# Performance work log

Measured on AMD Instinct MI355X. Metric: run time of the kernel, lower is better.

Reference implementation:

```python
import jax, jax.numpy as jnp
import numpy as np

B, N, E = 32, 2000, 32000      # graphs, nodes/graph, edges/graph
V, D, R, K = 100000, 128, 39, 8  # vocab, emb_dim, n_relation, n_bases
EPS = 1e-5


def setup_inputs() -> dict:
    key = jax.random.key(0)
    ks = jax.random.split(key, 8)
    node_ids = jax.random.randint(ks[0], (B, N), 0, V)
    edge_index = jax.random.randint(ks[1], (B, 2, E), 0, N)
    edge_type = jax.random.randint(ks[2], (B, E), 0, R)
    embedding = jax.random.normal(ks[3], (V, D), jnp.float32) * D ** -0.5
    bases = jax.random.normal(ks[4], (K, D, D), jnp.float32) * D ** -0.5
    comp = jax.random.normal(ks[5], (R, K), jnp.float32) * K ** -0.5
    root = jax.random.normal(ks[6], (D, D), jnp.float32) * D ** -0.5
    bias = jnp.zeros((D,), jnp.float32)
    return dict(node_ids=node_ids, edge_index=edge_index, edge_type=edge_type,
                embedding=embedding, bases=bases, comp=comp, root=root, bias=bias)


def _graph_fwd(node_ids, edge_index, edge_type, embedding, bases, comp, root, bias):
    # RGCNConv with basis decomposition and per-relation MEAN aggregation (PyG default).
    x = embedding[node_ids]                       # [N, D] per-graph node features
    src, dst = edge_index[0], edge_index[1]       # j -> i, aggregate at dst
    x_src = x[src]                                # [E, D]
    # mean normalizer per (dst, relation) bucket
    comb = dst * R + edge_type                    # [E]
    cnt = jax.ops.segment_sum(jnp.ones((E,), jnp.float32), comb, num_segments=N * R)
    inv = jnp.where(cnt > 0, 1.0 / cnt, 0.0)[comb]  # [E]
    # W_r = sum_k comp[r,k] * bases[k]; fold comp coefficients + mean norm into edge weights
    w = comp[edge_type] * inv[:, None]            # [E, K]
    out = x @ root + bias                         # root/self connection
    for k in range(K):                            # small fixed loop over bases
        zk = jax.ops.segment_sum(w[:, k:k + 1] * x_src, dst, num_segments=N)  # [N, D]
        out = out + zk @ bases[k]
    g = out.sum(axis=0)                           # sum pool over nodes
    # torch.nn.functional.normalize(p=2, eps=1e-5)
    return g / jnp.maximum(jnp.linalg.norm(g), EPS)


def reference(node_ids, edge_index, edge_type, embedding, bases, comp, root, bias):
    f = jax.vmap(_graph_fwd, in_axes=(0, 0, 0, None, None, None, None, None))
    return f(node_ids, edge_index, edge_type, embedding, bases, comp, root, bias)  # [B, D]
```

## Files before the change

### kernel.cpp

```cpp
#include <hip/hip_runtime.h>
#include <math.h>

#define Bn 32
#define Nn 2000
#define En 32000
#define Vn 100000
#define Dn 128
#define Rn 39
#define Kn 8

#define SUBS 8
#define NPS (Nn / SUBS)
#define WPG 64
#define NPAIR (Nn / 2)
#define EQ (En / 4)
#define NR (NPS * Rn)


__global__ __launch_bounds__(1024) void cntinv_kernel(const int* __restrict__ edge_index,
                                                      const int* __restrict__ edge_type,
                                                      float* __restrict__ inv) {
    int b = blockIdx.x, sub = blockIdx.y;
    int base = sub * NR;
    __shared__ int loc[NR];
    for (int i = threadIdx.x; i < NR; i += 1024) loc[i] = 0;
    __syncthreads();
    const int4* dst4 = (const int4*)(edge_index + (b * 2 + 1) * En);
    const int4* et4  = (const int4*)(edge_type + b * En);
    for (int q = threadIdx.x; q < EQ; q += 1024) {
        int4 d = dst4[q]; int4 t = et4[q]; int y;
        y = d.x * Rn + t.x - base; if ((unsigned)y < NR) atomicAdd(&loc[y], 1);
        y = d.y * Rn + t.y - base; if ((unsigned)y < NR) atomicAdd(&loc[y], 1);
        y = d.z * Rn + t.z - base; if ((unsigned)y < NR) atomicAdd(&loc[y], 1);
        y = d.w * Rn + t.w - base; if ((unsigned)y < NR) atomicAdd(&loc[y], 1);
    }
    __syncthreads();
    float* ivb = inv + (size_t)b * En;
    for (int q = threadIdx.x; q < EQ; q += 1024) {
        int4 d = dst4[q]; int4 t = et4[q];
        int e = 4 * q, y;
        y = d.x * Rn + t.x - base; if ((unsigned)y < NR) ivb[e]     = 1.0f / (float)loc[y];
        y = d.y * Rn + t.y - base; if ((unsigned)y < NR) ivb[e + 1] = 1.0f / (float)loc[y];
        y = d.z * Rn + t.z - base; if ((unsigned)y < NR) ivb[e + 2] = 1.0f / (float)loc[y];
        y = d.w * Rn + t.w - base; if ((unsigned)y < NR) ivb[e + 3] = 1.0f / (float)loc[y];
    }
}

__global__ __launch_bounds__(1024) void a_kernel(const int* __restrict__ edge_index,
                                                 const int* __restrict__ edge_type,
                                                 const float* __restrict__ inv,
                                                 const float* __restrict__ comp,
                                                 float* __restrict__ a) {
    int b = blockIdx.x, sub = blockIdx.y;
    int base = sub * NR;
    __shared__ float s[NR];
    __shared__ float comp_l[Rn * Kn];
    for (int i = threadIdx.x; i < NR; i += 1024) s[i] = 0.0f;
    if (threadIdx.x < Rn * Kn) comp_l[threadIdx.x] = comp[threadIdx.x];
    __syncthreads();
    const int4*   src4 = (const int4*)(edge_index + (b * 2 + 0) * En);
    const int4*   et4  = (const int4*)(edge_type + b * En);
    const float4* iv4  = (const float4*)(inv + (size_t)b * En);
    for (int q = threadIdx.x; q < EQ; q += 1024) {
        int4 sv = src4[q]; int4 tv = et4[q]; float4 iv = iv4[q]; int y;
        y = sv.x * Rn + tv.x - base; if ((unsigned)y < NR) atomicAdd(&s[y], iv.x);
        y = sv.y * Rn + tv.y - base; if ((unsigned)y < NR) atomicAdd(&s[y], iv.y);
        y = sv.z * Rn + tv.z - base; if ((unsigned)y < NR) atomicAdd(&s[y], iv.z);
        y = sv.w * Rn + tv.w - base; if ((unsigned)y < NR) atomicAdd(&s[y], iv.w);
    }
    __syncthreads();
    float* g = a + ((size_t)b * Nn + sub * NPS) * Kn;
    for (int i = threadIdx.x; i < NPS * Kn; i += 1024) {
        int n = i >> 3, k = i & 7;
        float acc = 0.0f;
        const float* srow = &s[n * Rn];
        for (int t = 0; t < Rn; t++) acc += srow[t] * comp_l[t * Kn + k];
        g[i] = acc;
    }
}

__global__ __launch_bounds__(256) void gather_kernel(const int* __restrict__ node_ids,
                                                     const float* __restrict__ emb,
                                                     const float* __restrict__ a,
                                                     float* __restrict__ partial) {
    int b = blockIdx.x;
    int lane = threadIdx.x & 63, wv = threadIdx.x >> 6;
    int W = blockIdx.y * 4 + wv;
    int half = lane >> 5;
    int dl = lane & 31;
    float4 acc[9];
#pragma unroll
    for (int k = 0; k < 9; k++) acc[k] = make_float4(0.f, 0.f, 0.f, 0.f);
    const int*   nb = node_ids + b * Nn;
    const float* ab = a + (size_t)b * Nn * Kn;
    for (int p0 = W; p0 < NPAIR; p0 += 8 * WPG) {
        bool   has[8];
        int    node[8];
        float4 v[8];
        float4 a0[8], a1[8];
#pragma unroll
        for (int i = 0; i < 8; i++) {
            int p = p0 + i * WPG;
            has[i] = p < NPAIR;
            node[i] = (has[i] ? 2 * p : 0) + half;
        }
#pragma unroll
        for (int i = 0; i < 8; i++) {
            int nid = nb[node[i]];
            v[i] = has[i] ? ((const float4*)(emb + (size_t)nid * Dn))[dl]
                          : make_float4(0.f, 0.f, 0.f, 0.f);
            const float4* ar = (const float4*)(ab + (size_t)node[i] * Kn);
            a0[i] = ar[0]; a1[i] = ar[1];
        }
#pragma unroll
        for (int i = 0; i < 8; i++) {
            float w[9] = {a0[i].x, a0[i].y, a0[i].z, a0[i].w,
                          a1[i].x, a1[i].y, a1[i].z, a1[i].w, 1.0f};
#pragma unroll
            for (int k = 0; k < 9; k++) {
                acc[k].x += w[k] * v[i].x;
                acc[k].y += w[k] * v[i].y;
                acc[k].z += w[k] * v[i].z;
                acc[k].w += w[k] * v[i].w;
            }
        }
    }
#pragma unroll
    for (int k = 0; k < 9; k++) {
        acc[k].x += __shfl_down(acc[k].x, 32, 64);
        acc[k].y += __shfl_down(acc[k].y, 32, 64);
        acc[k].z += __shfl_down(acc[k].z, 32, 64);
        acc[k].w += __shfl_down(acc[k].w, 32, 64);
    }
    if (half == 0) {
#pragma unroll
        for (int k = 0; k < 9; k++) {
            float4* gp = (float4*)(partial + (((size_t)b * 9 + k) * WPG + W) * Dn);
            gp[dl] = acc[k];
        }
    }
}

__global__ __launch_bounds__(256) void matvec_kernel(const float* __restrict__ partial,
                                                     const float* __restrict__ root,
                                                     const float* __restrict__ bases,
                                                     float* __restrict__ gmat) {
    int b = blockIdx.x, m = blockIdx.y;
    int tid = threadIdx.x;
    __shared__ float4 ts4[Dn / 4];
    __shared__ float tsh[8][Dn];
    int dg = tid & 31, part = tid >> 5;
    const float4* p4 = (const float4*)(partial + ((size_t)b * 9 + m) * WPG * Dn);
    float4 sum = make_float4(0.f, 0.f, 0.f, 0.f);
    for (int c = part; c < WPG; c += 8) {
        float4 v = p4[c * 32 + dg];
        sum.x += v.x; sum.y += v.y; sum.z += v.z; sum.w += v.w;
    }
    ((float4*)tsh[part])[dg] = sum;
    __syncthreads();
    if (part == 0) {
        float4 t = make_float4(0.f, 0.f, 0.f, 0.f);
#pragma unroll
        for (int r = 0; r < 8; r++) {
            float4 v = ((float4*)tsh[r])[dg];
            t.x += v.x; t.y += v.y; t.z += v.z; t.w += v.w;
        }
        ts4[dg] = t;
    }
    __syncthreads();
    const float* ts = (const float*)ts4;
    const float* M  = (m == 8) ? root : bases + (size_t)m * Dn * Dn;
    int d = tid & (Dn - 1), h = tid >> 7;
    float g = 0.0f;
    for (int j = h * 64; j < h * 64 + 64; j++) g += ts[j] * M[j * Dn + d];
    __syncthreads();
    tsh[h][d] = g;
    __syncthreads();
    if (h == 0) gmat[((size_t)b * 9 + m) * Dn + d] = tsh[0][d] + tsh[1][d];
}

__global__ __launch_bounds__(128) void norm_kernel(const float* __restrict__ gmat,
                                                   const float* __restrict__ bias,
                                                   float* __restrict__ out) {
    int b = blockIdx.x, d = threadIdx.x;
    float g = (float)Nn * bias[d];
    const float* gb = gmat + (size_t)b * 9 * Dn + d;
#pragma unroll
    for (int m = 0; m < 9; m++) g += gb[m * Dn];
    float ss = g * g;
#pragma unroll
    for (int off = 32; off > 0; off >>= 1) ss += __shfl_down(ss, off, 64);
    __shared__ float s2[2];
    if ((threadIdx.x & 63) == 0) s2[threadIdx.x >> 6] = ss;
    __syncthreads();
    float nrm = sqrtf(s2[0] + s2[1]);
    out[b * Dn + d] = g / fmaxf(nrm, 1e-5f);
}

extern "C" void kernel_launch(void* const* d_in, const int* in_sizes, int n_in,
                              void* d_out, int out_size, void* d_ws, size_t ws_size,
                              hipStream_t stream) {
    const int*   node_ids   = (const int*)d_in[0];
    const int*   edge_index = (const int*)d_in[1];
    const int*   edge_type  = (const int*)d_in[2];
    const float* embedding  = (const float*)d_in[3];
    const float* bases      = (const float*)d_in[4];
    const float* comp       = (const float*)d_in[5];
    const float* root       = (const float*)d_in[6];
    const float* bias       = (const float*)d_in[7];
    float*       out        = (float*)d_out;

    char* w = (char*)d_ws;
    float* inv     = (float*)(w + 0);
    float* a       = (float*)(w + 4096000);
    float* partial = (float*)(w + 6144000);
    float* gmat    = (float*)(w + 15581184);

    cntinv_kernel<<<dim3(Bn, SUBS),    1024, 0, stream>>>(edge_index, edge_type, inv);
    a_kernel     <<<dim3(Bn, SUBS),    1024, 0, stream>>>(edge_index, edge_type, inv, comp, a);
    gather_kernel<<<dim3(Bn, WPG / 4), 256,  0, stream>>>(node_ids, embedding, a, partial);
    matvec_kernel<<<dim3(Bn, 9),       256,  0, stream>>>(partial, root, bases, gmat);
    norm_kernel  <<<Bn, 128, 0, stream>>>(gmat, bias, out);
}
```

Measured before the change: 146.5 us.

## Reduce gather partials in shared memory and precompute inverse counts

The gather kernel now runs 512-thread blocks with 8 waves. Each block reduces its per-wave accumulators in shared memory and writes one partial per block, so the matvec stage reads 16 partials per graph instead of 64. The count kernel converts counts to reciprocals once per bucket in shared memory rather than dividing per edge, and the matvec inner loop is unrolled. This cuts partial-buffer traffic and division work, in exchange for a block-wide sync and a larger shared-memory footprint in the gather kernel.

```diff
diff --git a/kernel.cpp b/kernel.cpp
--- a/kernel.cpp
+++ b/kernel.cpp
@@ -11,10 +11,11 @@
 
 #define SUBS 8
 #define NPS (Nn / SUBS)
-#define WPG 64
 #define NPAIR (Nn / 2)
 #define EQ (En / 4)
 #define NR (NPS * Rn)
+#define GBLK 16
+#define WSLOT (GBLK * 8)
 
 
 __global__ __launch_bounds__(1024) void cntinv_kernel(const int* __restrict__ edge_index,
@@ -35,14 +36,20 @@
         y = d.w * Rn + t.w - base; if ((unsigned)y < NR) atomicAdd(&loc[y], 1);
     }
     __syncthreads();
+    float* finv = (float*)loc;
+    for (int i = threadIdx.x; i < NR; i += 1024) {
+        int c = loc[i];
+        finv[i] = 1.0f / (float)c;
+    }
+    __syncthreads();
     float* ivb = inv + (size_t)b * En;
     for (int q = threadIdx.x; q < EQ; q += 1024) {
         int4 d = dst4[q]; int4 t = et4[q];
         int e = 4 * q, y;
-        y = d.x * Rn + t.x - base; if ((unsigned)y < NR) ivb[e]     = 1.0f / (float)loc[y];
-        y = d.y * Rn + t.y - base; if ((unsigned)y < NR) ivb[e + 1] = 1.0f / (float)loc[y];
-        y = d.z * Rn + t.z - base; if ((unsigned)y < NR) ivb[e + 2] = 1.0f / (float)loc[y];
-        y = d.w * Rn + t.w - base; if ((unsigned)y < NR) ivb[e + 3] = 1.0f / (float)loc[y];
+        y = d.x * Rn + t.x - base; if ((unsigned)y < NR) ivb[e]     = finv[y];
+        y = d.y * Rn + t.y - base; if ((unsigned)y < NR) ivb[e + 1] = finv[y];
+        y = d.z * Rn + t.z - base; if ((unsigned)y < NR) ivb[e + 2] = finv[y];
+        y = d.w * Rn + t.w - base; if ((unsigned)y < NR) ivb[e + 3] = finv[y];
     }
 }
 
@@ -79,33 +86,35 @@
     }
 }
 
-__global__ __launch_bounds__(256) void gather_kernel(const int* __restrict__ node_ids,
-                                                     const float* __restrict__ emb,
-                                                     const float* __restrict__ a,
-                                                     float* __restrict__ partial) {
+__global__ __launch_bounds__(512, 4) void gather_kernel(const int* __restrict__ node_ids,
+                                                        const float* __restrict__ emb,
+                                                        const float* __restrict__ a,
+                                                        float* __restrict__ partial) {
     int b = blockIdx.x;
     int lane = threadIdx.x & 63, wv = threadIdx.x >> 6;
-    int W = blockIdx.y * 4 + wv;
+    int Wl = blockIdx.y * 8 + wv;
     int half = lane >> 5;
     int dl = lane & 31;
+    __shared__ float red[8][9][Dn];
     float4 acc[9];
 #pragma unroll
     for (int k = 0; k < 9; k++) acc[k] = make_float4(0.f, 0.f, 0.f, 0.f);
     const int*   nb = node_ids + b * Nn;
     const float* ab = a + (size_t)b * Nn * Kn;
-    for (int p0 = W; p0 < NPAIR; p0 += 8 * WPG) {
-        bool   has[8];
-        int    node[8];
-        float4 v[8];
-        float4 a0[8], a1[8];
-#pragma unroll
-        for (int i = 0; i < 8; i++) {
-            int p = p0 + i * WPG;
+#pragma unroll
+    for (int i0 = 0; i0 < 8; i0 += 4) {
+        bool   has[4];
+        int    node[4];
+        float4 v[4];
+        float4 a0[4], a1[4];
+#pragma unroll
+        for (int i = 0; i < 4; i++) {
+            int p = Wl + (i0 + i) * WSLOT;
             has[i] = p < NPAIR;
             node[i] = (has[i] ? 2 * p : 0) + half;
         }
 #pragma unroll
-        for (int i = 0; i < 8; i++) {
+        for (int i = 0; i < 4; i++) {
             int nid = nb[node[i]];
             v[i] = has[i] ? ((const float4*)(emb + (size_t)nid * Dn))[dl]
                           : make_float4(0.f, 0.f, 0.f, 0.f);
@@ -113,7 +122,7 @@
             a0[i] = ar[0]; a1[i] = ar[1];
         }
 #pragma unroll
-        for (int i = 0; i < 8; i++) {
+        for (int i = 0; i < 4; i++) {
             float w[9] = {a0[i].x, a0[i].y, a0[i].z, a0[i].w,
                           a1[i].x, a1[i].y, a1[i].z, a1[i].w, 1.0f};
 #pragma unroll
@@ -134,10 +143,21 @@
     }
     if (half == 0) {
 #pragma unroll
-        for (int k = 0; k < 9; k++) {
-            float4* gp = (float4*)(partial + (((size_t)b * 9 + k) * WPG + W) * Dn);
-            gp[dl] = acc[k];
-        }
+        for (int k = 0; k < 9; k++)
+            ((float4*)red[wv][k])[dl] = acc[k];
+    }
+    __syncthreads();
+    int slot = threadIdx.x;
+    if (slot < 9 * (Dn / 4)) {
+        int k = slot >> 5, d4 = slot & 31;
+        float4 t = make_float4(0.f, 0.f, 0.f, 0.f);
+#pragma unroll
+        for (int w = 0; w < 8; w++) {
+            float4 v = ((const float4*)red[w][k])[d4];
+            t.x += v.x; t.y += v.y; t.z += v.z; t.w += v.w;
+        }
+        float4* gp = (float4*)(partial + (((size_t)b * 9 + k) * GBLK + blockIdx.y) * Dn);
+        gp[d4] = t;
     }
 }
 
@@ -150,9 +170,9 @@
     __shared__ float4 ts4[Dn / 4];
     __shared__ float tsh[8][Dn];
     int dg = tid & 31, part = tid >> 5;
-    const float4* p4 = (const float4*)(partial + ((size_t)b * 9 + m) * WPG * Dn);
+    const float4* p4 = (const float4*)(partial + ((size_t)b * 9 + m) * GBLK * Dn);
     float4 sum = make_float4(0.f, 0.f, 0.f, 0.f);
-    for (int c = part; c < WPG; c += 8) {
+    for (int c = part; c < GBLK; c += 8) {
         float4 v = p4[c * 32 + dg];
         sum.x += v.x; sum.y += v.y; sum.z += v.z; sum.w += v.w;
     }
@@ -172,6 +192,7 @@
     const float* M  = (m == 8) ? root : bases + (size_t)m * Dn * Dn;
     int d = tid & (Dn - 1), h = tid >> 7;
     float g = 0.0f;
+#pragma unroll 8
     for (int j = h * 64; j < h * 64 + 64; j++) g += ts[j] * M[j * Dn + d];
     __syncthreads();
     tsh[h][d] = g;
@@ -214,11 +235,11 @@
     float* inv     = (float*)(w + 0);
     float* a       = (float*)(w + 4096000);
     float* partial = (float*)(w + 6144000);
-    float* gmat    = (float*)(w + 15581184);
-
-    cntinv_kernel<<<dim3(Bn, SUBS),    1024, 0, stream>>>(edge_index, edge_type, inv);
-    a_kernel     <<<dim3(Bn, SUBS),    1024, 0, stream>>>(edge_index, edge_type, inv, comp, a);
-    gather_kernel<<<dim3(Bn, WPG / 4), 256,  0, stream>>>(node_ids, embedding, a, partial);
-    matvec_kernel<<<dim3(Bn, 9),       256,  0, stream>>>(partial, root, bases, gmat);
+    float* gmat    = (float*)(w + 8503296);
+
+    cntinv_kernel<<<dim3(Bn, SUBS), 1024, 0, stream>>>(edge_index, edge_type, inv);
+    a_kernel     <<<dim3(Bn, SUBS), 1024, 0, stream>>>(edge_index, edge_type, inv, comp, a);
+    gather_kernel<<<dim3(Bn, GBLK), 512,  0, stream>>>(node_ids, embedding, a, partial);
+    matvec_kernel<<<dim3(Bn, 9),    256,  0, stream>>>(partial, root, bases, gmat);
     norm_kernel  <<<Bn, 128, 0, stream>>>(gmat, bias, out);
 }
```

Result: faster. 141.4 us (median of 2 runs) (-3.5%).
